# Optimization experiments

Measured on AMD Instinct MI355X. Metric: run time of the kernel, lower is better.

The kernel has to match this reference:

```python
import jax, jax.numpy as jnp
import numpy as np

N = 50000   # nodes
E = 640000  # edges
D = 128     # hidden_size
BN_EPS = 1e-5


def _bn(x, g, b):
    # BatchNorm1d, training-mode batch statistics (biased variance), per-feature
    m = jnp.mean(x, axis=0)
    v = jnp.var(x, axis=0)
    return g * (x - m) * jax.lax.rsqrt(v + BN_EPS) + b


def _gin_mlp(x, W1, b1, g, bb, W2, b2):
    # Linear -> BatchNorm1d -> GELU(exact) -> Linear
    h = jax.nn.gelu(_bn(x @ W1 + b1, g, bb), approximate=False)
    return h @ W2 + b2


def _ffn(x, W1, b1, g1, bb1, W2, b2, g2, bb2):
    # fc1=(Linear+BN) -> GELU -> fc2=(Linear+BN) -> +shortcut
    h = jax.nn.gelu(_bn(x @ W1 + b1, g1, bb1), approximate=False)
    return _bn(h @ W2 + b2, g2, bb2) + x


def setup_inputs() -> dict:
    key = jax.random.key(0)
    ks = iter(jax.random.split(key, 16))

    def p(*s):
        return jax.random.normal(next(ks), s, jnp.float32) * 0.05

    inp = {
        "x": jax.random.normal(next(ks), (N, D), jnp.float32),
        "edge_index": jax.random.randint(next(ks), (2, E), 0, N, jnp.int32),
        # node_encoder + batch_norm
        "enc_W": p(D, D), "enc_b": jnp.zeros(D, jnp.float32),
        "bn_g": jnp.ones(D, jnp.float32), "bn_b": jnp.zeros(D, jnp.float32),
        # GINConv MLP: Linear(D,D)+BN+GELU+Linear(D,D)
        "gW1": p(D, D), "gb1": jnp.zeros(D, jnp.float32),
        "gg": jnp.ones(D, jnp.float32), "gbb": jnp.zeros(D, jnp.float32),
        "gW2": p(D, D), "gb2": jnp.zeros(D, jnp.float32),
        # fc2 = FFN(D, 2D)
        "f2W1": p(D, 2 * D), "f2b1": jnp.zeros(2 * D, jnp.float32),
        "f2g1": jnp.ones(2 * D, jnp.float32), "f2bb1": jnp.zeros(2 * D, jnp.float32),
        "f2W2": p(2 * D, D), "f2b2": jnp.zeros(D, jnp.float32),
        "f2g2": jnp.ones(D, jnp.float32), "f2bb2": jnp.zeros(D, jnp.float32),
        # ffn = FFN(D, 4D)
        "fnW1": p(D, 4 * D), "fnb1": jnp.zeros(4 * D, jnp.float32),
        "fng1": jnp.ones(4 * D, jnp.float32), "fnbb1": jnp.zeros(4 * D, jnp.float32),
        "fnW2": p(4 * D, D), "fnb2": jnp.zeros(D, jnp.float32),
        "fng2": jnp.ones(D, jnp.float32), "fnbb2": jnp.zeros(D, jnp.float32),
    }
    return inp


def reference(x, edge_index, enc_W, enc_b, bn_g, bn_b,
              gW1, gb1, gg, gbb, gW2, gb2,
              f2W1, f2b1, f2g1, f2bb1, f2W2, f2b2, f2g2, f2bb2,
              fnW1, fnb1, fng1, fnbb1, fnW2, fnb2, fng2, fnbb2):
    shortcut = x
    # node_encoder + BN
    h = _bn(x @ enc_W + enc_b, bn_g, bn_b)  # [N, D]
    # GINConv: out = MLP((1+eps)*h + sum_{j->i} h_j), eps=0
    src, dst = edge_index[0], edge_index[1]
    agg = jax.ops.segment_sum(h[src], dst, num_segments=N)  # scatter-add [N, D]
    h = _gin_mlp(h + agg, gW1, gb1, gg, gbb, gW2, gb2)
    # fc2 FFN (hidden 2D, internal residual)
    h = _ffn(h, f2W1, f2b1, f2g1, f2bb1, f2W2, f2b2, f2g2, f2bb2)
    # outer residual
    h = shortcut + h
    # final FFN (hidden 4D, internal residual)
    return _ffn(h, fnW1, fnb1, fng1, fnbb1, fnW2, fnb2, fng2, fnbb2)
```

## Files before the change

### kernel.cpp

```cpp
#include <hip/hip_runtime.h>
#include <hip/hip_bf16.h>

typedef __attribute__((ext_vector_type(8))) short short8;
typedef __attribute__((ext_vector_type(4))) float f32x4;

__device__ __forceinline__ float bf2f(unsigned short u) {
    union { unsigned int i; float f; } c;
    c.i = ((unsigned int)u) << 16;
    return c.f;
}
__device__ __forceinline__ unsigned short f2bf(float f) {
    union { float f; unsigned int i; } c;
    c.f = f;
    unsigned int x = c.i;
    x += 0x7FFFu + ((x >> 16) & 1u);
    return (unsigned short)(x >> 16);
}
__device__ __forceinline__ float gelu_fast(float x) {
    const float x2 = x * x;
    const float t = x * fmaf(0.0713548163f, x2, 1.5957691216f);
    const float e = __expf(t);
    const float r = __builtin_amdgcn_rcpf(e + 1.0f);
    return fmaf(-x, r, x);
}

#define NPART 64

template<int K, int M, int XF>
__global__ __launch_bounds__(256, (K > 256) ? 4 : 5)
void gemmf_kernel(const void* __restrict__ Av,
                  const float* __restrict__ pCoef,
                  const unsigned short* __restrict__ Wp,
                  const float* __restrict__ bias,
                  float* __restrict__ part,
                  unsigned short* __restrict__ C,
                  int nrows)
{
    constexpr int KS_TOT = K / 32;
    constexpr int NKC    = K / 128;
    constexpr int NCT    = M / 128;
    constexpr bool DBUF  = (K > 256);
    constexpr int NFRAG  = DBUF ? 32 : 4 * KS_TOT;
    __shared__ __align__(16) char smem[NFRAG * 1024 + ((NCT > 1) ? 16384 : 0)];
    char* cbuf = smem + ((NCT > 1) ? NFRAG * 1024 : 0);

    const int tid = threadIdx.x;
    const int l   = tid & 63, wv = tid >> 6;
    const int gr0 = blockIdx.x * 64;
    const int kq4 = l & 3, rloc = l >> 2;
    const int woff = ((kq4 * 16 + rloc) * 16) ^ (kq4 << 5);
    const int loff = (l * 16) ^ ((l >> 4) << 5);

    int rowg[4];
    #pragma unroll
    for (int i = 0; i < 4; ++i) {
        int rg = gr0 + i * 16 + rloc;
        rowg[i] = rg < nrows ? rg : nrows - 1;
    }

    f32x4 acc[4][2];
    short8 breg[2][4];

    auto loadB = [&](int ct, int kcb) {
        #pragma unroll
        for (int c = 0; c < 2; ++c) {
            const int col = ct * 128 + (wv * 2 + c) * 16 + (l & 15);
            const unsigned short* bp = Wp + (size_t)col * K + kcb + (l >> 4) * 8;
            #pragma unroll
            for (int ks = 0; ks < 4; ++ks)
                breg[c][ks] = *(const short8*)(bp + ks * 32);
        }
    };

    auto xf2 = [&](short8 t, const float* sc8, const float* sh8) -> short8 {
        short8 val;
        #pragma unroll
        for (int j = 0; j < 8; ++j) {
            float v = fmaf(sc8[j], bf2f((unsigned short)t[j]), sh8[j]);
            val[j] = (short)f2bf(gelu_fast(v));
        }
        return val;
    };

    auto epilogue = [&](int ct) {
        const int lrow = l & 15, kg = l >> 4;
        __syncthreads();
        #pragma unroll
        for (int c = 0; c < 2; ++c) {
            const int col  = (wv * 2 + c) * 16 + lrow;
            const int gcol = ct * 128 + col;
            const float bc = bias[gcol];
            float s = 0.f, q = 0.f;
            #pragma unroll
            for (int r = 0; r < 4; ++r) {
                #pragma unroll
                for (int i = 0; i < 4; ++i) {
                    const int rl = r * 16 + kg * 4 + i;
                    const float v = acc[r][c][i] + bc;
                    if (gr0 + rl < nrows) { s += v; q += v * v; }
                    const int byte = rl * 256 + ((col * 2) ^ ((rl & 7) << 4));
                    *(unsigned short*)(cbuf + byte) = f2bf(v);
                }
            }
            s += __shfl_xor(s, 16); s += __shfl_xor(s, 32);
            q += __shfl_xor(q, 16); q += __shfl_xor(q, 32);
            if (kg == 0 && part != nullptr) {
                float* ps = part + (size_t)(blockIdx.x & (NPART - 1)) * (2 * M);
                atomicAdd(&ps[gcol], s);
                atomicAdd(&ps[M + gcol], q);
            }
        }
        __syncthreads();
        #pragma unroll
        for (int j = 0; j < 4; ++j) {
            const int lin = j * 256 + tid;
            const int rl = lin >> 4, chunk = lin & 15;
            const int row = gr0 + rl;
            if (row < nrows) {
                short8 vv = *(const short8*)(cbuf + rl * 256 + ((chunk * 16) ^ ((rl & 7) << 4)));
                *(short8*)(C + (size_t)row * M + ct * 128 + chunk * 8) = vv;
            }
        }
    };

    if constexpr (!DBUF) {
        #pragma unroll
        for (int h = 0; h < NKC; ++h) {
            const int kst = h * 4 + wv;
            const int c0k = kst * 32 + kq4 * 8;
            float sc8[8], sh8[8];
            if (XF == 2) {
                #pragma unroll
                for (int j = 0; j < 8; ++j) {
                    sc8[j] = pCoef[c0k + j];
                    sh8[j] = pCoef[K + c0k + j];
                }
            }
            #pragma unroll
            for (int i = 0; i < 4; ++i) {
                const size_t eoff = (size_t)rowg[i] * K + c0k;
                short8 val;
                if (XF == 0) {
                    val = *(const short8*)((const unsigned short*)Av + eoff);
                } else if (XF == 1) {
                    const float* A = (const float*)Av;
                    f32x4 u0 = *(const f32x4*)(A + eoff);
                    f32x4 u1 = *(const f32x4*)(A + eoff + 4);
                    #pragma unroll
                    for (int j = 0; j < 4; ++j) {
                        val[j]     = (short)f2bf(u0[j]);
                        val[j + 4] = (short)f2bf(u1[j]);
                    }
                } else {
                    short8 t = *(const short8*)((const unsigned short*)Av + eoff);
                    val = xf2(t, sc8, sh8);
                }
                *(short8*)(smem + (i * KS_TOT + kst) * 1024 + woff) = val;
            }
        }
        __syncthreads();
        #pragma unroll
        for (int ct = 0; ct < NCT; ++ct) {
            #pragma unroll
            for (int r = 0; r < 4; ++r)
                #pragma unroll
                for (int c = 0; c < 2; ++c) acc[r][c] = f32x4{0.f, 0.f, 0.f, 0.f};
            #pragma unroll
            for (int kc = 0; kc < NKC; ++kc) {
                loadB(ct, kc * 128);
                #pragma unroll
                for (int ks = 0; ks < 4; ++ks) {
                    const int ksg = kc * 4 + ks;
                    short8 af[4];
                    #pragma unroll
                    for (int r = 0; r < 4; ++r)
                        af[r] = *(const short8*)(smem + (r * KS_TOT + ksg) * 1024 + loff);
                    #pragma unroll
                    for (int r = 0; r < 4; ++r)
                        #pragma unroll
                        for (int c = 0; c < 2; ++c)
                            acc[r][c] = __builtin_amdgcn_mfma_f32_16x16x32_bf16(af[r], breg[c][ks], acc[r][c], 0, 0, 0);
                }
            }
            epilogue(ct);
        }
    } else {
        const int akoff = wv * 32 + kq4 * 8;
        auto stageChunk = [&](int kcb, int b, const short8* pre) {
            const int c0k = kcb + akoff;
            float sc8[8], sh8[8];
            if (XF == 2) {
                #pragma unroll
                for (int j = 0; j < 8; ++j) {
                    sc8[j] = pCoef[c0k + j];
                    sh8[j] = pCoef[K + c0k + j];
                }
            }
            #pragma unroll
            for (int i = 0; i < 4; ++i) {
                short8 t = pre ? pre[i]
                              : *(const short8*)((const unsigned short*)Av + (size_t)rowg[i] * K + c0k);
                short8 val = (XF == 2) ? xf2(t, sc8, sh8) : t;
                *(short8*)(smem + (b * 16 + i * 4 + wv) * 1024 + woff) = val;
            }
        };
        stageChunk(0, 0, nullptr);
        __syncthreads();
        #pragma unroll
        for (int r = 0; r < 4; ++r)
            #pragma unroll
            for (int c = 0; c < 2; ++c) acc[r][c] = f32x4{0.f, 0.f, 0.f, 0.f};
        #pragma unroll
        for (int kc = 0; kc < NKC; ++kc) {
            const int cur = kc & 1;
            loadB(0, kc * 128);
            short8 anext[4];
            if (kc + 1 < NKC) {
                const int c0k = (kc + 1) * 128 + akoff;
                #pragma unroll
                for (int i = 0; i < 4; ++i)
                    anext[i] = *(const short8*)((const unsigned short*)Av + (size_t)rowg[i] * K + c0k);
            }
            #pragma unroll
            for (int ks = 0; ks < 4; ++ks) {
                short8 af[4];
                #pragma unroll
                for (int r = 0; r < 4; ++r)
                    af[r] = *(const short8*)(smem + (cur * 16 + r * 4 + ks) * 1024 + loff);
                #pragma unroll
                for (int r = 0; r < 4; ++r)
                    #pragma unroll
                    for (int c = 0; c < 2; ++c)
                        acc[r][c] = __builtin_amdgcn_mfma_f32_16x16x32_bf16(af[r], breg[c][ks], acc[r][c], 0, 0, 0);
            }
            if (kc + 1 < NKC) {
                stageChunk((kc + 1) * 128, cur ^ 1, anext);
                __syncthreads();
            }
        }
        epilogue(0);
    }
}

__global__ void coef_kernel(const float* __restrict__ part,
                            const float* __restrict__ g, const float* __restrict__ b,
                            float* __restrict__ scsh, int W, float invN)
{
    int i = blockIdx.x * blockDim.x + threadIdx.x;
    if (i >= W) return;
    float s = 0.f, q = 0.f;
    #pragma unroll 8
    for (int r = 0; r < NPART; ++r) {
        s += part[(size_t)r * 2 * W + i];
        q += part[(size_t)r * 2 * W + W + i];
    }
    const float mean = s * invN;
    const float var  = q * invN - mean * mean;
    const float sc   = g[i] * rsqrtf(var + 1e-5f);
    scsh[i] = sc;
    scsh[W + i] = b[i] - mean * sc;
}

__global__ void h3_kernel(const unsigned short* __restrict__ t4,
                          const float* __restrict__ coef,
                          const unsigned short* __restrict__ t2,
                          const float* __restrict__ xr,
                          unsigned short* __restrict__ H3, int total4)
{
    int idx = blockIdx.x * blockDim.x + threadIdx.x;
    if (idx >= total4) return;
    const int base = idx * 4;
    const int c0 = base & 127;
    ushort4 tv = *(const ushort4*)(t4 + base);
    ushort4 uv = *(const ushort4*)(t2 + base);
    float4  xv = *(const float4*)(xr + base);
    unsigned short ts[4] = {tv.x, tv.y, tv.z, tv.w};
    unsigned short us[4] = {uv.x, uv.y, uv.z, uv.w};
    const float* px = &xv.x;
    ushort4 ov;
    unsigned short* po = &ov.x;
    #pragma unroll
    for (int j = 0; j < 4; ++j) {
        const int c = c0 + j;
        po[j] = f2bf(fmaf(coef[c], bf2f(ts[j]), coef[128 + c]) + bf2f(us[j]) + px[j]);
    }
    *(ushort4*)(H3 + base) = ov;
}

__global__ void hist_kernel(const int* __restrict__ ei, int* __restrict__ cnt, int E)
{
    int e = blockIdx.x * blockDim.x + threadIdx.x;
    if (e < E) atomicAdd(&cnt[ei[E + e]], 1);
}

__global__ void scan_reduce(const int* __restrict__ cnt, int* __restrict__ blksum, int n)
{
    __shared__ int s[256];
    int t = threadIdx.x;
    int i = blockIdx.x * 256 + t;
    s[t] = i < n ? cnt[i] : 0;
    __syncthreads();
    for (int d = 128; d > 0; d >>= 1) {
        if (t < d) s[t] += s[t + d];
        __syncthreads();
    }
    if (t == 0) blksum[blockIdx.x] = s[0];
}

__global__ void scan_top(int* __restrict__ blksum, int nb)
{
    __shared__ int s[256];
    int t = threadIdx.x;
    int v = t < nb ? blksum[t] : 0;
    s[t] = v;
    __syncthreads();
    for (int d = 1; d < 256; d <<= 1) {
        int u = (t >= d) ? s[t - d] : 0;
        __syncthreads();
        s[t] += u;
        __syncthreads();
    }
    if (t < nb) blksum[t] = s[t] - v;
}

__global__ void scan_apply(const int* __restrict__ cnt, const int* __restrict__ blksum,
                           int* __restrict__ offs, int* __restrict__ cursor, int n)
{
    __shared__ int s[256];
    int t = threadIdx.x;
    int i = blockIdx.x * 256 + t;
    int v = i < n ? cnt[i] : 0;
    s[t] = v;
    __syncthreads();
    for (int d = 1; d < 256; d <<= 1) {
        int u = (t >= d) ? s[t - d] : 0;
        __syncthreads();
        s[t] += u;
        __syncthreads();
    }
    int excl = s[t] - v + blksum[blockIdx.x];
    if (i < n) { offs[i] = excl; cursor[i] = excl; }
}

__global__ void place_kernel(const int* __restrict__ ei, int* __restrict__ cursor,
                             int* __restrict__ ssrc, int E)
{
    int e = blockIdx.x * blockDim.x + threadIdx.x;
    if (e < E) {
        int pos = atomicAdd(&cursor[ei[E + e]], 1);
        ssrc[pos] = ei[e];
    }
}

__global__ __launch_bounds__(256)
void gather_kernel(const unsigned short* __restrict__ T0,
                   const float* __restrict__ coef,
                   const int* __restrict__ ssrc, const int* __restrict__ offs,
                   const int* __restrict__ cnt,
                   unsigned short* __restrict__ Zb, int N)
{
    const int wave = threadIdx.x >> 6;
    const int lane = threadIdx.x & 63;
    const int node = blockIdx.x * 4 + wave;
    if (node >= N) return;

    unsigned int hv = *(const unsigned int*)(T0 + (size_t)node * 128 + lane * 2);
    float a0 = bf2f((unsigned short)hv);
    float a1 = bf2f((unsigned short)(hv >> 16));

    const int off = offs[node];
    const int deg = cnt[node];
    for (int base = 0; base < deg; base += 64) {
        int m = deg - base;
        if (m > 64) m = 64;
        int idx = (base + lane < deg) ? ssrc[off + base + lane] : 0;
        int k = 0;
        for (; k + 1 < m; k += 2) {
            int s0 = __shfl(idx, k);
            int s1 = __shfl(idx, k + 1);
            unsigned int v0 = *(const unsigned int*)(T0 + (size_t)s0 * 128 + lane * 2);
            unsigned int v1 = *(const unsigned int*)(T0 + (size_t)s1 * 128 + lane * 2);
            a0 += bf2f((unsigned short)v0) + bf2f((unsigned short)v1);
            a1 += bf2f((unsigned short)(v0 >> 16)) + bf2f((unsigned short)(v1 >> 16));
        }
        if (k < m) {
            int s0 = __shfl(idx, k);
            unsigned int v0 = *(const unsigned int*)(T0 + (size_t)s0 * 128 + lane * 2);
            a0 += bf2f((unsigned short)v0);
            a1 += bf2f((unsigned short)(v0 >> 16));
        }
    }
    const int c0 = lane * 2;
    const float dp1 = (float)(deg + 1);
    const float z0 = fmaf(coef[c0], a0, dp1 * coef[128 + c0]);
    const float z1 = fmaf(coef[c0 + 1], a1, dp1 * coef[128 + c0 + 1]);
    unsigned int o = ((unsigned int)f2bf(z1) << 16) | (unsigned int)f2bf(z0);
    *(unsigned int*)(Zb + (size_t)node * 128 + lane * 2) = o;
}

__global__ void final_kernel(const unsigned short* __restrict__ t6,
                             const float* __restrict__ coef,
                             const unsigned short* __restrict__ h3,
                             float* __restrict__ out, int total4)
{
    int idx = blockIdx.x * blockDim.x + threadIdx.x;
    if (idx >= total4) return;
    const int base = idx * 4;
    const int c0 = base & 127;
    ushort4 tv = *(const ushort4*)(t6 + base);
    ushort4 hv = *(const ushort4*)(h3 + base);
    unsigned short ts[4] = {tv.x, tv.y, tv.z, tv.w};
    unsigned short hs[4] = {hv.x, hv.y, hv.z, hv.w};
    float4 ov;
    float* po = &ov.x;
    #pragma unroll
    for (int j = 0; j < 4; ++j) {
        const int c = c0 + j;
        po[j] = fmaf(coef[c], bf2f(ts[j]), coef[128 + c]) + bf2f(hs[j]);
    }
    *(float4*)(out + base) = ov;
}

struct PackDesc { const float* src; unsigned short* dst; int K; int M; };
struct Pack7 { PackDesc d[7]; };
__global__ void pack_kernel(Pack7 p)
{
    PackDesc d = p.d[blockIdx.y];
    const int total = d.K * d.M;
    for (int idx = blockIdx.x * blockDim.x + threadIdx.x; idx < total;
         idx += gridDim.x * blockDim.x) {
        const int k = idx / d.M;
        const int m = idx - k * d.M;
        d.dst[(size_t)m * d.K + k] = f2bf(d.src[idx]);
    }
}

extern "C" void kernel_launch(void* const* d_in, const int* in_sizes, int n_in,
                              void* d_out, int out_size, void* d_ws, size_t ws_size,
                              hipStream_t stream)
{
    const float* x     = (const float*)d_in[0];
    const int*   ei    = (const int*)d_in[1];
    const float* enc_W = (const float*)d_in[2];
    const float* enc_b = (const float*)d_in[3];
    const float* bn_g  = (const float*)d_in[4];
    const float* bn_b  = (const float*)d_in[5];
    const float* gW1   = (const float*)d_in[6];
    const float* gb1   = (const float*)d_in[7];
    const float* gg    = (const float*)d_in[8];
    const float* gbb   = (const float*)d_in[9];
    const float* gW2   = (const float*)d_in[10];
    const float* gb2   = (const float*)d_in[11];
    const float* f2W1  = (const float*)d_in[12];
    const float* f2b1  = (const float*)d_in[13];
    const float* f2g1  = (const float*)d_in[14];
    const float* f2bb1 = (const float*)d_in[15];
    const float* f2W2  = (const float*)d_in[16];
    const float* f2b2  = (const float*)d_in[17];
    const float* f2g2  = (const float*)d_in[18];
    const float* f2bb2 = (const float*)d_in[19];
    const float* fnW1  = (const float*)d_in[20];
    const float* fnb1  = (const float*)d_in[21];
    const float* fng1  = (const float*)d_in[22];
    const float* fnbb1 = (const float*)d_in[23];
    const float* fnW2  = (const float*)d_in[24];
    const float* fnb2  = (const float*)d_in[25];
    const float* fng2  = (const float*)d_in[26];
    const float* fnbb2 = (const float*)d_in[27];

    const int D = 128;
    const int N = in_sizes[0] / D;
    const int E = in_sizes[1] / 2;
    const float invN = 1.0f / (float)N;

    char* w = (char*)d_ws;
    float* c0 = (float*)w;
    float* c1 = c0 + 256;
    float* c3 = c1 + 256;
    float* c4 = c3 + 512;
    float* c5 = c4 + 256;
    float* c6 = c5 + 1024;
    const size_t coefBytes = 2560 * sizeof(float);
    size_t off = coefBytes;

    float* p0 = (float*)(w + off); off += (size_t)NPART * 256 * 4;
    float* p1 = (float*)(w + off); off += (size_t)NPART * 256 * 4;
    float* p3 = (float*)(w + off); off += (size_t)NPART * 512 * 4;
    float* p4 = (float*)(w + off); off += (size_t)NPART * 256 * 4;
    float* p5 = (float*)(w + off); off += (size_t)NPART * 1024 * 4;
    float* p6 = (float*)(w + off); off += (size_t)NPART * 256 * 4;
    const size_t partBytes = (size_t)NPART * 2560 * 4;

    unsigned short* wpE  = (unsigned short*)(w + off); off += (size_t)128 * 128 * 2;
    unsigned short* wpG1 = (unsigned short*)(w + off); off += (size_t)128 * 128 * 2;
    unsigned short* wpG2 = (unsigned short*)(w + off); off += (size_t)128 * 128 * 2;
    unsigned short* wpF1 = (unsigned short*)(w + off); off += (size_t)128 * 256 * 2;
    unsigned short* wpF2 = (unsigned short*)(w + off); off += (size_t)256 * 128 * 2;
    unsigned short* wpN1 = (unsigned short*)(w + off); off += (size_t)128 * 512 * 2;
    unsigned short* wpN2 = (unsigned short*)(w + off); off += (size_t)512 * 128 * 2;

    unsigned short* P1 = (unsigned short*)(w + off); off += (size_t)N * 128 * 2;
    unsigned short* Zb = (unsigned short*)(w + off); off += (size_t)N * 128 * 2;
    unsigned short* H3 = (unsigned short*)(w + off); off += (size_t)N * 128 * 2;
    unsigned short* T3 = (unsigned short*)(w + off); off += (size_t)N * 256 * 2;
    unsigned short* T5 = (unsigned short*)(w + off); off += (size_t)N * 512 * 2;

    const int NB = (N + 255) / 256;
    char* csr = (char*)T5;
    int* cnt    = (int*)csr;  csr += (size_t)NB * 256 * 4;
    int* offs   = (int*)csr;  csr += (size_t)NB * 256 * 4;
    int* cursor = (int*)csr;  csr += (size_t)NB * 256 * 4;
    int* blksum = (int*)csr;  csr += 1024;
    int* ssrc   = (int*)csr;

    hipMemsetAsync(p0, 0, partBytes, stream);
    hipMemsetAsync(cnt, 0, (size_t)NB * 256 * 4, stream);

    Pack7 pk;
    pk.d[0] = PackDesc{enc_W, wpE, 128, 128};
    pk.d[1] = PackDesc{gW1, wpG1, 128, 128};
    pk.d[2] = PackDesc{gW2, wpG2, 128, 128};
    pk.d[3] = PackDesc{f2W1, wpF1, 128, 256};
    pk.d[4] = PackDesc{f2W2, wpF2, 256, 128};
    pk.d[5] = PackDesc{fnW1, wpN1, 128, 512};
    pk.d[6] = PackDesc{fnW2, wpN2, 512, 128};
    pack_kernel<<<dim3(64, 7), 256, 0, stream>>>(pk);

    const int eb = (E + 255) / 256;
    hist_kernel<<<eb, 256, 0, stream>>>(ei, cnt, E);
    scan_reduce<<<NB, 256, 0, stream>>>(cnt, blksum, N);
    scan_top<<<1, 256, 0, stream>>>(blksum, NB);
    scan_apply<<<NB, 256, 0, stream>>>(cnt, blksum, offs, cursor, N);
    place_kernel<<<eb, 256, 0, stream>>>(ei, cursor, ssrc, E);

    const int rb  = (N + 63) / 64;
    const int t4a = N * 128 / 4;
    const int ewb = (t4a + 255) / 256;

    gemmf_kernel<128, 128, 1><<<rb, 256, 0, stream>>>(
        x, nullptr, wpE, enc_b, p0, P1, N);
    coef_kernel<<<1, 256, 0, stream>>>(p0, bn_g, bn_b, c0, 128, invN);
    gather_kernel<<<(N + 3) / 4, 256, 0, stream>>>(
        P1, c0, ssrc, offs, cnt, Zb, N);
    gemmf_kernel<128, 128, 0><<<rb, 256, 0, stream>>>(
        Zb, nullptr, wpG1, gb1, p1, P1, N);
    coef_kernel<<<1, 256, 0, stream>>>(p1, gg, gbb, c1, 128, invN);
    gemmf_kernel<128, 128, 2><<<rb, 256, 0, stream>>>(
        P1, c1, wpG2, gb2, nullptr, Zb, N);
    gemmf_kernel<128, 256, 0><<<rb, 256, 0, stream>>>(
        Zb, nullptr, wpF1, f2b1, p3, T3, N);
    coef_kernel<<<1, 256, 0, stream>>>(p3, f2g1, f2bb1, c3, 256, invN);
    gemmf_kernel<256, 128, 2><<<rb, 256, 0, stream>>>(
        T3, c3, wpF2, f2b2, p4, P1, N);
    coef_kernel<<<1, 256, 0, stream>>>(p4, f2g2, f2bb2, c4, 128, invN);
    h3_kernel<<<ewb, 256, 0, stream>>>(P1, c4, Zb, x, H3, t4a);
    gemmf_kernel<128, 512, 0><<<rb, 256, 0, stream>>>(
        H3, nullptr, wpN1, fnb1, p5, T5, N);
    coef_kernel<<<2, 256, 0, stream>>>(p5, fng1, fnbb1, c5, 512, invN);
    gemmf_kernel<512, 128, 2><<<rb, 256, 0, stream>>>(
        T5, c5, wpN2, fnb2, p6, P1, N);
    coef_kernel<<<1, 256, 0, stream>>>(p6, fng2, fnbb2, c6, 128, invN);
    final_kernel<<<ewb, 256, 0, stream>>>(P1, c6, H3, (float*)d_out, t4a);

    (void)n_in; (void)out_size; (void)ws_size;
}
```

Before: 318.2 us.

## Fuse h3 residual into FFN GEMM, merge pack/hist and encoder/place kernels

Folds the h3 elementwise kernel (BN apply, two residual adds, bf16 cast) into the A-staging of the 128->512 GEMM, which also writes H3 out for the final residual. Merges the weight-pack and histogram launches into one grid, and runs the CSR place step inside the same grid as the encoder GEMM using extra blocks. This removes three launches and one full read/write pass over the N x 128 activations. The cost is extra global loads in the FFN1 staging and a larger, heterogeneous encoder grid.

```diff
diff --git a/kernel.cpp b/kernel.cpp
--- a/kernel.cpp
+++ b/kernel.cpp
@@ -30,6 +30,9 @@
 __global__ __launch_bounds__(256, (K > 256) ? 4 : 5)
 void gemmf_kernel(const void* __restrict__ Av,
                   const float* __restrict__ pCoef,
+                  const unsigned short* __restrict__ res1,
+                  const float* __restrict__ res2,
+                  unsigned short* __restrict__ h3out,
                   const unsigned short* __restrict__ Wp,
                   const float* __restrict__ bias,
                   float* __restrict__ part,
@@ -52,10 +55,12 @@
     const int loff = (l * 16) ^ ((l >> 4) << 5);
 
     int rowg[4];
+    bool rval[4];
     #pragma unroll
     for (int i = 0; i < 4; ++i) {
         int rg = gr0 + i * 16 + rloc;
-        rowg[i] = rg < nrows ? rg : nrows - 1;
+        rval[i] = rg < nrows;
+        rowg[i] = rval[i] ? rg : nrows - 1;
     }
 
     f32x4 acc[4][2];
@@ -129,7 +134,7 @@
             const int kst = h * 4 + wv;
             const int c0k = kst * 32 + kq4 * 8;
             float sc8[8], sh8[8];
-            if (XF == 2) {
+            if (XF >= 2) {
                 #pragma unroll
                 for (int j = 0; j < 8; ++j) {
                     sc8[j] = pCoef[c0k + j];
@@ -151,9 +156,21 @@
                         val[j]     = (short)f2bf(u0[j]);
                         val[j + 4] = (short)f2bf(u1[j]);
                     }
+                } else if (XF == 2) {
+                    short8 t = *(const short8*)((const unsigned short*)Av + eoff);
+                    val = xf2(t, sc8, sh8);
                 } else {
                     short8 t = *(const short8*)((const unsigned short*)Av + eoff);
-                    val = xf2(t, sc8, sh8);
+                    short8 u = *(const short8*)(res1 + eoff);
+                    f32x4 x0 = *(const f32x4*)(res2 + eoff);
+                    f32x4 x1 = *(const f32x4*)(res2 + eoff + 4);
+                    #pragma unroll
+                    for (int j = 0; j < 8; ++j) {
+                        float v = fmaf(sc8[j], bf2f((unsigned short)t[j]), sh8[j]);
+                        v += bf2f((unsigned short)u[j]) + ((j < 4) ? x0[j] : x1[j - 4]);
+                        val[j] = (short)f2bf(v);
+                    }
+                    if (rval[i]) *(short8*)(h3out + eoff) = val;
                 }
                 *(short8*)(smem + (i * KS_TOT + kst) * 1024 + woff) = val;
             }
@@ -189,7 +206,7 @@
         auto stageChunk = [&](int kcb, int b, const short8* pre) {
             const int c0k = kcb + akoff;
             float sc8[8], sh8[8];
-            if (XF == 2) {
+            if (XF >= 2) {
                 #pragma unroll
                 for (int j = 0; j < 8; ++j) {
                     sc8[j] = pCoef[c0k + j];
@@ -239,6 +256,115 @@
             }
         }
         epilogue(0);
+    }
+}
+
+__global__ __launch_bounds__(256, 5)
+void enc_place_kernel(const float* __restrict__ Av,
+                      const unsigned short* __restrict__ Wp,
+                      const float* __restrict__ bias,
+                      float* __restrict__ part,
+                      unsigned short* __restrict__ C, int nrows, int rb,
+                      const int* __restrict__ ei, int* __restrict__ cursor,
+                      int* __restrict__ ssrc, int E)
+{
+    __shared__ __align__(16) char smem[16384];
+    if ((int)blockIdx.x >= rb) {
+        const int e = (blockIdx.x - rb) * 256 + threadIdx.x;
+        if (e < E) {
+            int pos = atomicAdd(&cursor[ei[E + e]], 1);
+            ssrc[pos] = ei[e];
+        }
+        return;
+    }
+    const int tid = threadIdx.x;
+    const int l = tid & 63, wv = tid >> 6;
+    const int gr0 = blockIdx.x * 64;
+    const int kq4 = l & 3, rloc = l >> 2;
+    const int woff = ((kq4 * 16 + rloc) * 16) ^ (kq4 << 5);
+    const int loff = (l * 16) ^ ((l >> 4) << 5);
+    const int lrow = l & 15, kg = l >> 4;
+    const int akoff = wv * 32 + kq4 * 8;
+
+    int rowg[4];
+    #pragma unroll
+    for (int i = 0; i < 4; ++i) {
+        int rg = gr0 + i * 16 + rloc;
+        rowg[i] = rg < nrows ? rg : nrows - 1;
+    }
+    #pragma unroll
+    for (int i = 0; i < 4; ++i) {
+        const float* p = Av + (size_t)rowg[i] * 128 + akoff;
+        f32x4 u0 = *(const f32x4*)p;
+        f32x4 u1 = *(const f32x4*)(p + 4);
+        short8 val;
+        #pragma unroll
+        for (int j = 0; j < 4; ++j) {
+            val[j]     = (short)f2bf(u0[j]);
+            val[j + 4] = (short)f2bf(u1[j]);
+        }
+        *(short8*)(smem + (i * 4 + wv) * 1024 + woff) = val;
+    }
+    __syncthreads();
+
+    short8 breg[2][4];
+    #pragma unroll
+    for (int c = 0; c < 2; ++c) {
+        const int col = (wv * 2 + c) * 16 + lrow;
+        const unsigned short* bp = Wp + (size_t)col * 128 + kg * 8;
+        #pragma unroll
+        for (int ks = 0; ks < 4; ++ks) breg[c][ks] = *(const short8*)(bp + ks * 32);
+    }
+    f32x4 acc[4][2];
+    #pragma unroll
+    for (int r = 0; r < 4; ++r)
+        #pragma unroll
+        for (int c = 0; c < 2; ++c) acc[r][c] = f32x4{0.f, 0.f, 0.f, 0.f};
+    #pragma unroll
+    for (int ks = 0; ks < 4; ++ks) {
+        short8 af[4];
+        #pragma unroll
+        for (int r = 0; r < 4; ++r)
+            af[r] = *(const short8*)(smem + (r * 4 + ks) * 1024 + loff);
+        #pragma unroll
+        for (int r = 0; r < 4; ++r)
+            #pragma unroll
+            for (int c = 0; c < 2; ++c)
+                acc[r][c] = __builtin_amdgcn_mfma_f32_16x16x32_bf16(af[r], breg[c][ks], acc[r][c], 0, 0, 0);
+    }
+    __syncthreads();
+    #pragma unroll
+    for (int c = 0; c < 2; ++c) {
+        const int col = (wv * 2 + c) * 16 + lrow;
+        const float bc = bias[col];
+        float s = 0.f, q = 0.f;
+        #pragma unroll
+        for (int r = 0; r < 4; ++r)
+            #pragma unroll
+            for (int i = 0; i < 4; ++i) {
+                const int rl = r * 16 + kg * 4 + i;
+                const float v = acc[r][c][i] + bc;
+                if (gr0 + rl < nrows) { s += v; q += v * v; }
+                *(unsigned short*)(smem + rl * 256 + ((col * 2) ^ ((rl & 7) << 4))) = f2bf(v);
+            }
+        s += __shfl_xor(s, 16); s += __shfl_xor(s, 32);
+        q += __shfl_xor(q, 16); q += __shfl_xor(q, 32);
+        if (kg == 0) {
+            float* ps = part + (size_t)(blockIdx.x & (NPART - 1)) * 256;
+            atomicAdd(&ps[col], s);
+            atomicAdd(&ps[128 + col], q);
+        }
+    }
+    __syncthreads();
+    #pragma unroll
+    for (int j = 0; j < 4; ++j) {
+        const int lin = j * 256 + tid;
+        const int rl = lin >> 4, chunk = lin & 15;
+        const int row = gr0 + rl;
+        if (row < nrows) {
+            short8 vv = *(const short8*)(smem + rl * 256 + ((chunk * 16) ^ ((rl & 7) << 4)));
+            *(short8*)(C + (size_t)row * 128 + chunk * 8) = vv;
+        }
     }
 }
 
@@ -261,36 +387,24 @@
     scsh[W + i] = b[i] - mean * sc;
 }
 
-__global__ void h3_kernel(const unsigned short* __restrict__ t4,
-                          const float* __restrict__ coef,
-                          const unsigned short* __restrict__ t2,
-                          const float* __restrict__ xr,
-                          unsigned short* __restrict__ H3, int total4)
-{
-    int idx = blockIdx.x * blockDim.x + threadIdx.x;
-    if (idx >= total4) return;
-    const int base = idx * 4;
-    const int c0 = base & 127;
-    ushort4 tv = *(const ushort4*)(t4 + base);
-    ushort4 uv = *(const ushort4*)(t2 + base);
-    float4  xv = *(const float4*)(xr + base);
-    unsigned short ts[4] = {tv.x, tv.y, tv.z, tv.w};
-    unsigned short us[4] = {uv.x, uv.y, uv.z, uv.w};
-    const float* px = &xv.x;
-    ushort4 ov;
-    unsigned short* po = &ov.x;
-    #pragma unroll
-    for (int j = 0; j < 4; ++j) {
-        const int c = c0 + j;
-        po[j] = f2bf(fmaf(coef[c], bf2f(ts[j]), coef[128 + c]) + bf2f(us[j]) + px[j]);
-    }
-    *(ushort4*)(H3 + base) = ov;
-}
-
-__global__ void hist_kernel(const int* __restrict__ ei, int* __restrict__ cnt, int E)
-{
-    int e = blockIdx.x * blockDim.x + threadIdx.x;
-    if (e < E) atomicAdd(&cnt[ei[E + e]], 1);
+struct PackDesc { const float* src; unsigned short* dst; int K; int M; };
+struct Pack7 { PackDesc d[7]; };
+__global__ void pack_hist_kernel(Pack7 p, const int* __restrict__ ei,
+                                 int* __restrict__ cnt, int E)
+{
+    if (blockIdx.x < 448) {
+        const PackDesc d = p.d[blockIdx.x >> 6];
+        const int total = d.K * d.M;
+        for (int idx = (blockIdx.x & 63) * 256 + threadIdx.x; idx < total;
+             idx += 64 * 256) {
+            const int k = idx / d.M;
+            const int m = idx - k * d.M;
+            d.dst[(size_t)m * d.K + k] = f2bf(d.src[idx]);
+        }
+    } else {
+        const int e = (blockIdx.x - 448) * 256 + threadIdx.x;
+        if (e < E) atomicAdd(&cnt[ei[E + e]], 1);
+    }
 }
 
 __global__ void scan_reduce(const int* __restrict__ cnt, int* __restrict__ blksum, int n)
@@ -340,16 +454,6 @@
     }
     int excl = s[t] - v + blksum[blockIdx.x];
     if (i < n) { offs[i] = excl; cursor[i] = excl; }
-}
-
-__global__ void place_kernel(const int* __restrict__ ei, int* __restrict__ cursor,
-                             int* __restrict__ ssrc, int E)
-{
-    int e = blockIdx.x * blockDim.x + threadIdx.x;
-    if (e < E) {
-        int pos = atomicAdd(&cursor[ei[E + e]], 1);
-        ssrc[pos] = ei[e];
-    }
 }
 
 __global__ __launch_bounds__(256)
@@ -419,20 +523,6 @@
         po[j] = fmaf(coef[c], bf2f(ts[j]), coef[128 + c]) + bf2f(hs[j]);
     }
     *(float4*)(out + base) = ov;
-}
-
-struct PackDesc { const float* src; unsigned short* dst; int K; int M; };
-struct Pack7 { PackDesc d[7]; };
-__global__ void pack_kernel(Pack7 p)
-{
-    PackDesc d = p.d[blockIdx.y];
-    const int total = d.K * d.M;
-    for (int idx = blockIdx.x * blockDim.x + threadIdx.x; idx < total;
-         idx += gridDim.x * blockDim.x) {
-        const int k = idx / d.M;
-        const int m = idx - k * d.M;
-        d.dst[(size_t)m * d.K + k] = f2bf(d.src[idx]);
-    }
 }
 
 extern "C" void kernel_launch(void* const* d_in, const int* in_sizes, int n_in,
@@ -524,41 +614,38 @@
     pk.d[4] = PackDesc{f2W2, wpF2, 256, 128};
     pk.d[5] = PackDesc{fnW1, wpN1, 128, 512};
     pk.d[6] = PackDesc{fnW2, wpN2, 512, 128};
-    pack_kernel<<<dim3(64, 7), 256, 0, stream>>>(pk);
 
     const int eb = (E + 255) / 256;
-    hist_kernel<<<eb, 256, 0, stream>>>(ei, cnt, E);
+    const int rb = (N + 63) / 64;
+    const int t4a = N * 128 / 4;
+    const int ewb = (t4a + 255) / 256;
+
+    pack_hist_kernel<<<448 + eb, 256, 0, stream>>>(pk, ei, cnt, E);
     scan_reduce<<<NB, 256, 0, stream>>>(cnt, blksum, N);
     scan_top<<<1, 256, 0, stream>>>(blksum, NB);
     scan_apply<<<NB, 256, 0, stream>>>(cnt, blksum, offs, cursor, N);
-    place_kernel<<<eb, 256, 0, stream>>>(ei, cursor, ssrc, E);
-
-    const int rb  = (N + 63) / 64;
-    const int t4a = N * 128 / 4;
-    const int ewb = (t4a + 255) / 256;
-
-    gemmf_kernel<128, 128, 1><<<rb, 256, 0, stream>>>(
-        x, nullptr, wpE, enc_b, p0, P1, N);
+
+    enc_place_kernel<<<rb + eb, 256, 0, stream>>>(
+        x, wpE, enc_b, p0, P1, N, rb, ei, cursor, ssrc, E);
     coef_kernel<<<1, 256, 0, stream>>>(p0, bn_g, bn_b, c0, 128, invN);
     gather_kernel<<<(N + 3) / 4, 256, 0, stream>>>(
         P1, c0, ssrc, offs, cnt, Zb, N);
     gemmf_kernel<128, 128, 0><<<rb, 256, 0, stream>>>(
-        Zb, nullptr, wpG1, gb1, p1, P1, N);
+        Zb, nullptr, nullptr, nullptr, nullptr, wpG1, gb1, p1, P1, N);
     coef_kernel<<<1, 256, 0, stream>>>(p1, gg, gbb, c1, 128, invN);
     gemmf_kernel<128, 128, 2><<<rb, 256, 0, stream>>>(
-        P1, c1, wpG2, gb2, nullptr, Zb, N);
+        P1, c1, nullptr, nullptr, nullptr, wpG2, gb2, nullptr, Zb, N);
     gemmf_kernel<128, 256, 0><<<rb, 256, 0, stream>>>(
-        Zb, nullptr, wpF1, f2b1, p3, T3, N);
+        Zb, nullptr, nullptr, nullptr, nullptr, wpF1, f2b1, p3, T3, N);
     coef_kernel<<<1, 256, 0, stream>>>(p3, f2g1, f2bb1, c3, 256, invN);
     gemmf_kernel<256, 128, 2><<<rb, 256, 0, stream>>>(
-        T3, c3, wpF2, f2b2, p4, P1, N);
+        T3, c3, nullptr, nullptr, nullptr, wpF2, f2b2, p4, P1, N);
     coef_kernel<<<1, 256, 0, stream>>>(p4, f2g2, f2bb2, c4, 128, invN);
-    h3_kernel<<<ewb, 256, 0, stream>>>(P1, c4, Zb, x, H3, t4a);
-    gemmf_kernel<128, 512, 0><<<rb, 256, 0, stream>>>(
-        H3, nullptr, wpN1, fnb1, p5, T5, N);
+    gemmf_kernel<128, 512, 3><<<rb, 256, 0, stream>>>(
+        P1, c4, Zb, x, H3, wpN1, fnb1, p5, T5, N);
     coef_kernel<<<2, 256, 0, stream>>>(p5, fng1, fnbb1, c5, 512, invN);
     gemmf_kernel<512, 128, 2><<<rb, 256, 0, stream>>>(
-        T5, c5, wpN2, fnb2, p6, P1, N);
+        T5, c5, nullptr, nullptr, nullptr, wpN2, fnb2, p6, P1, N);
     coef_kernel<<<1, 256, 0, stream>>>(p6, fng2, fnbb2, c6, 128, invN);
     final_kernel<<<ewb, 256, 0, stream>>>(P1, c6, H3, (float*)d_out, t4a);
 
```

After: 313.1 us. Within noise of the previous version (-1.6%).
